# Performance work log

Hardware: AMD Instinct MI355X
Metric: run time of the kernel (lower is better)

## Reference

```python
import jax, jax.numpy as jnp
import numpy as np
import math

DIM = 1024
H = 16            # num_heads
HD = DIM // H // 2  # 32, per-split head dim
DEPTH = 4
LAMBDA_INIT = 0.8 - 0.6 * math.exp(-0.3 * DEPTH)
SCALE = HD ** -0.5
EPS = 1e-5


def setup_inputs() -> dict:
    key = jax.random.key(0)
    ks = jax.random.split(key, 12)
    B, Nq, Nk = 2, 2048, 2048
    s = DIM ** -0.5
    return {
        "query": jax.random.normal(ks[0], (B, Nq, DIM), jnp.float32),
        "key_": jax.random.normal(ks[1], (B, Nk, DIM), jnp.float32),
        "value": jax.random.normal(ks[2], (B, Nk, DIM), jnp.float32),
        "Wq": jax.random.normal(ks[3], (DIM, DIM), jnp.float32) * s,
        "Wk": jax.random.normal(ks[4], (DIM, DIM), jnp.float32) * s,
        "Wv": jax.random.normal(ks[5], (DIM, DIM), jnp.float32) * s,
        "Wp": jax.random.normal(ks[6], (DIM, DIM), jnp.float32) * s,
        "bp": jnp.zeros((DIM,), jnp.float32),
        "lq1": jax.random.normal(ks[7], (HD,), jnp.float32) * 0.1,
        "lk1": jax.random.normal(ks[8], (HD,), jnp.float32) * 0.1,
        "lq2": jax.random.normal(ks[9], (HD,), jnp.float32) * 0.1,
        "lk2": jax.random.normal(ks[10], (HD,), jnp.float32) * 0.1,
        "subln_w": jnp.ones((2 * HD,), jnp.float32),
    }


def _sdpa(q, k, v):
    # q,k: [B,H,Nq/Nk,HD], v: [B,H,Nk,2*HD]
    scores = jnp.einsum("bhqd,bhkd->bhqk", q * SCALE, k)
    p = jax.nn.softmax(scores, axis=-1)
    return jnp.einsum("bhqk,bhkd->bhqd", p, v)


def reference(query, key_, value, Wq, Wk, Wv, Wp, bp, lq1, lk1, lq2, lk2, subln_w):
    B, Nq, C = query.shape
    Nk = key_.shape[1]
    # projections (torch Linear: x @ W.T)
    q = (query @ Wq.T).reshape(B, Nq, 2 * H, HD).transpose(0, 2, 1, 3)  # [B,2H,Nq,HD]
    k = (key_ @ Wk.T).reshape(B, Nk, 2 * H, HD).transpose(0, 2, 1, 3)   # [B,2H,Nk,HD]
    v = (value @ Wv.T).reshape(B, Nk, H, 2 * HD).transpose(0, 2, 1, 3)  # [B,H,Nk,2HD]
    q1, q2 = q[:, :H], q[:, H:]
    k1, k2 = k[:, :H], k[:, H:]
    a1 = _sdpa(q1, k1, v)  # [B,H,Nq,2HD]
    a2 = _sdpa(q2, k2, v)
    lam1 = jnp.exp(jnp.sum(lq1 * lk1))
    lam2 = jnp.exp(jnp.sum(lq2 * lk2))
    lam = lam1 - lam2 + LAMBDA_INIT
    attn = a1 - lam * a2                       # [B,H,Nq,2HD]
    attn = attn.transpose(0, 2, 1, 3)          # [B,Nq,H,2HD]
    # RMSNorm over last dim
    attn = attn * jax.lax.rsqrt(jnp.mean(attn * attn, axis=-1, keepdims=True) + EPS)
    attn = attn * subln_w
    attn = attn * (1.0 - LAMBDA_INIT)
    attn = attn.reshape(B, Nq, C)
    return attn @ Wp.T + bp
```

## Files before the change

kernel.cpp:

```cpp
#include <hip/hip_runtime.h>

using u16 = unsigned short;
using u32 = unsigned int;
typedef __attribute__((ext_vector_type(8))) short bf16x8;
typedef __attribute__((ext_vector_type(4))) float f32x4;
typedef __attribute__((ext_vector_type(4))) float f4;

#define DIMC 1024
#define NQ 2048
#define NK 2048

static constexpr float LAMBDA_INIT = 0.6192834728526787f;
static constexpr float ONE_MINUS_LI = 1.0f - 0.6192834728526787f;
static constexpr float SCALE_ = 0.17677669529663687f;
static constexpr float LOG2E_ = 1.4426950408889634f;
static constexpr float EPS_ = 1e-5f;

__device__ __forceinline__ u16 f2bf(float f) {
    union { float f; unsigned u; } v; v.f = f;
    unsigned u = v.u;
    unsigned r = (u + 0x7FFFu + ((u >> 16) & 1u)) >> 16;
    return (u16)r;
}

__device__ __forceinline__ u32 packbf_trunc(float a, float b) {
    return (__float_as_uint(a) >> 16) | (__float_as_uint(b) & 0xFFFF0000u);
}

__device__ __forceinline__ void gload_lds16(const u16* g, u16* l) {
    __builtin_amdgcn_global_load_lds(
        (const __attribute__((address_space(1))) unsigned int*)g,
        (__attribute__((address_space(3))) unsigned int*)l,
        16, 0, 0);
}

__global__ __launch_bounds__(256) void cvt_all_kernel(
    const float* __restrict__ q, const float* __restrict__ k, const float* __restrict__ v,
    const float* __restrict__ wq, const float* __restrict__ wk,
    const float* __restrict__ wv, const float* __restrict__ wp,
    u16* __restrict__ qo, u16* __restrict__ ko, u16* __restrict__ vo,
    u16* __restrict__ wqo, u16* __restrict__ wko, u16* __restrict__ wvo, u16* __restrict__ wpo)
{
    const int bid = blockIdx.x;
    const float* s; u16* d; int rb;
    if (bid < 6144) {
        const int r = bid >> 11;
        rb = bid & 2047;
        s = (r == 0) ? q : (r == 1) ? k : v;
        d = (r == 0) ? qo : (r == 1) ? ko : vo;
    } else {
        const int r = (bid - 6144) >> 9;
        rb = (bid - 6144) & 511;
        s = (r == 0) ? wq : (r == 1) ? wk : (r == 2) ? wv : wp;
        d = (r == 0) ? wqo : (r == 1) ? wko : (r == 2) ? wvo : wpo;
    }
    const size_t i = (size_t)rb * 2048 + threadIdx.x * 8;
    f4 a = *(const f4*)(s + i);
    f4 b = *(const f4*)(s + i + 4);
    bf16x8 r8;
    r8[0] = (short)f2bf(a[0]); r8[1] = (short)f2bf(a[1]);
    r8[2] = (short)f2bf(a[2]); r8[3] = (short)f2bf(a[3]);
    r8[4] = (short)f2bf(b[0]); r8[5] = (short)f2bf(b[1]);
    r8[6] = (short)f2bf(b[2]); r8[7] = (short)f2bf(b[3]);
    *(bf16x8*)(d + i) = r8;
}

template<int OUT_MODE>
__device__ __forceinline__ void gemm_tile(
    const u16* __restrict__ A, const u16* __restrict__ B,
    void* __restrict__ C, const float* __restrict__ bias,
    int tm, int tn, int N, float osc)
{
    constexpr int K = 1024;
    const int lane = threadIdx.x & 63;
    const int wave = threadIdx.x >> 6;
    const int wr = wave >> 1, wc = wave & 1;
    const int l15 = lane & 15, l4 = lane >> 4;
    const int arow0 = tm + wr * 64, brow0 = tn + wc * 64;

    const u16* Ab = A + (size_t)(arow0 + l15) * K + 8 * l4;
    const u16* Bb = B + (size_t)(brow0 + l15) * K + 8 * l4;

    f32x4 acc[4][4];
    f32x4 zf = {0.f, 0.f, 0.f, 0.f};
#pragma unroll
    for (int i = 0; i < 4; ++i)
#pragma unroll
        for (int j = 0; j < 4; ++j) acc[i][j] = zf;

#pragma unroll 2
    for (int k0 = 0; k0 < K; k0 += 32) {
        bf16x8 af[4], bfr[4];
#pragma unroll
        for (int i = 0; i < 4; ++i) af[i] = *(const bf16x8*)(Ab + (size_t)i * 16 * K + k0);
#pragma unroll
        for (int j = 0; j < 4; ++j) bfr[j] = *(const bf16x8*)(Bb + (size_t)j * 16 * K + k0);
#pragma unroll
        for (int i = 0; i < 4; ++i)
#pragma unroll
            for (int j = 0; j < 4; ++j)
                acc[i][j] = __builtin_amdgcn_mfma_f32_16x16x32_bf16(af[i], bfr[j], acc[i][j], 0, 0, 0);
    }

#pragma unroll
    for (int i = 0; i < 4; ++i)
#pragma unroll
        for (int j = 0; j < 4; ++j)
#pragma unroll
            for (int r = 0; r < 4; ++r) {
                const int row = arow0 + i * 16 + l4 * 4 + r;
                const int col = brow0 + j * 16 + l15;
                const float v = acc[i][j][r];
                if (OUT_MODE == 0)
                    ((u16*)C)[(size_t)row * N + col] = f2bf(v * osc);
                else
                    ((float*)C)[(size_t)row * N + col] = v + bias[col];
            }
}

__global__ __launch_bounds__(256) void qkv_gemm_kernel(
    const u16* __restrict__ qa, const u16* __restrict__ wq, u16* __restrict__ qo,
    const u16* __restrict__ ka, const u16* __restrict__ wk, u16* __restrict__ ko,
    const u16* __restrict__ wv, const u16* __restrict__ va, u16* __restrict__ vo,
    float qosc)
{
    int id = blockIdx.x + 8 * (blockIdx.y + 32 * blockIdx.z);
    id = (id & 7) * 96 + (id >> 3);
    const int x = id & 7, y = (id >> 3) & 31, z = id >> 8;

    if (z == 0)      gemm_tile<0>(qa, wq, qo, nullptr, y * 128, x * 128, 1024, qosc);
    else if (z == 1) gemm_tile<0>(ka, wk, ko, nullptr, y * 128, x * 128, 1024, 1.0f);
    else             gemm_tile<0>(wv, va, vo, nullptr, x * 128, y * 128, 4096, 1.0f);
}

__global__ __launch_bounds__(256) void out_gemm_kernel(
    const u16* __restrict__ A, const u16* __restrict__ Bw,
    float* __restrict__ C, const float* __restrict__ bias)
{
    int id = blockIdx.x + 8 * blockIdx.y;
    id = (id & 7) * 32 + (id >> 3);
    const int x = id & 7, y = id >> 3;
    gemm_tile<1>(A, Bw, C, bias, y * 128, x * 128, 1024, 1.0f);
}

__global__ __launch_bounds__(256) void attn_kernel(
    const u16* __restrict__ Qb, const u16* __restrict__ Kb, const u16* __restrict__ Vt,
    const float* __restrict__ lq1, const float* __restrict__ lk1,
    const float* __restrict__ lq2, const float* __restrict__ lk2,
    const float* __restrict__ subln, u16* __restrict__ X2)
{
    const int tid = threadIdx.x;
    const int lane = tid & 63;
    const int wv = tid >> 6;
    const int l15 = lane & 15, l4 = lane >> 4;

    int id = blockIdx.x;
    id = (id & 7) * 128 + (id >> 3);
    const int qt = id & 31, h = (id >> 5) & 15, b = id >> 9;
    const int q0 = qt * 64 + wv * 16;

    __shared__ alignas(16) u16 Kbuf[2][4096];
    __shared__ alignas(16) u16 Vbuf[2][4096];
    __shared__ alignas(16) u16 Ps[4][2][1024];
    u16* P1 = &Ps[wv][0][0];
    u16* P2 = &Ps[wv][1][0];

    float s1 = 0.f, s2 = 0.f;
#pragma unroll
    for (int i = 0; i < 32; ++i) { s1 += lq1[i] * lk1[i]; s2 += lq2[i] * lk2[i]; }
    const float lam = __expf(s1) - __expf(s2) + LAMBDA_INIT;

    const u16* Qbase = Qb + (size_t)b * NQ * DIMC;
    const u16* Krow = Kb + (size_t)b * NK * DIMC + (size_t)lane * DIMC + h * 32;
    const u16* Vrow = Vt + (size_t)h * 64 * 4096 + (size_t)b * 2048 + (size_t)lane * 4096;

    const bf16x8 q1f = *(const bf16x8*)(Qbase + (size_t)(q0 + l15) * DIMC + h * 32 + 8 * l4);
    const bf16x8 q2f = *(const bf16x8*)(Qbase + (size_t)(q0 + l15) * DIMC + 512 + h * 32 + 8 * l4);

    float m1 = -1e30f, d1 = 0.f, m2 = -1e30f, d2 = 0.f;
    f32x4 acc1[4], acc2[4];
    f32x4 zf = {0.f, 0.f, 0.f, 0.f};
#pragma unroll
    for (int t = 0; t < 4; ++t) { acc1[t] = zf; acc2[t] = zf; }

    const int wrow = l4 << 2;

    auto STAGE = [&](int nb, int kv) {
#pragma unroll
        for (int g = 0; g < 2; ++g) {
            const int c = g * 4 + wv;
            const int koff = (c < 4) ? c * 8 : 512 + (c - 4) * 8;
            gload_lds16(Krow + (size_t)kv * DIMC + koff, &Kbuf[nb][c * 512]);
            gload_lds16(Vrow + kv + c * 8,               &Vbuf[nb][c * 512]);
        }
    };

    STAGE(0, 0);
    __syncthreads();

    int buf = 0;
    for (int t = 0; t < 32; ++t) {
        if (t < 31) STAGE(buf ^ 1, (t + 1) * 64);

        const u16* Kl = &Kbuf[buf][0];
        const u16* Vl = &Vbuf[buf][0];

        f32x4 sc1[4], sc2[4];
#pragma unroll
        for (int s = 0; s < 4; ++s) {
            bf16x8 k1 = *(const bf16x8*)(Kl + l4 * 512 + (s * 16 + l15) * 8);
            bf16x8 k2 = *(const bf16x8*)(Kl + (4 + l4) * 512 + (s * 16 + l15) * 8);
            sc1[s] = __builtin_amdgcn_mfma_f32_16x16x32_bf16(k1, q1f, zf, 0, 0, 0);
            sc2[s] = __builtin_amdgcn_mfma_f32_16x16x32_bf16(k2, q2f, zf, 0, 0, 0);
        }

        {
            float pm = sc1[0][0];
#pragma unroll
            for (int s = 0; s < 4; ++s)
#pragma unroll
                for (int r = 0; r < 4; ++r) pm = fmaxf(pm, sc1[s][r]);
            pm = fmaxf(pm, __shfl_xor(pm, 16));
            pm = fmaxf(pm, __shfl_xor(pm, 32));
            if (!__all(pm - m1 <= 8.f)) {
                const float mnew = fmaxf(m1, pm);
                const float alpha = __builtin_amdgcn_exp2f(m1 - mnew);
                m1 = mnew;
                d1 *= alpha;
                float ar[4];
#pragma unroll
                for (int r = 0; r < 4; ++r) ar[r] = __shfl(alpha, wrow + r);
#pragma unroll
                for (int tt = 0; tt < 4; ++tt)
#pragma unroll
                    for (int r = 0; r < 4; ++r) acc1[tt][r] *= ar[r];
            }
            float rs = 0.f;
            float p[4][4];
#pragma unroll
            for (int s = 0; s < 4; ++s)
#pragma unroll
                for (int r = 0; r < 4; ++r) {
                    p[s][r] = __builtin_amdgcn_exp2f(sc1[s][r] - m1);
                    rs += p[s][r];
                }
            rs += __shfl_xor(rs, 16);
            rs += __shfl_xor(rs, 32);
            d1 += rs;
#pragma unroll
            for (int s = 0; s < 4; ++s) {
                uint2 wvv;
                wvv.x = packbf_trunc(p[s][0], p[s][1]);
                wvv.y = packbf_trunc(p[s][2], p[s][3]);
                const int idx = ((l15 << 6) + (s << 4) + (l4 << 2)) ^ ((l15 & 7) << 3);
                *(uint2*)&P1[idx] = wvv;
            }
        }
        {
            float pm = sc2[0][0];
#pragma unroll
            for (int s = 0; s < 4; ++s)
#pragma unroll
                for (int r = 0; r < 4; ++r) pm = fmaxf(pm, sc2[s][r]);
            pm = fmaxf(pm, __shfl_xor(pm, 16));
            pm = fmaxf(pm, __shfl_xor(pm, 32));
            if (!__all(pm - m2 <= 8.f)) {
                const float mnew = fmaxf(m2, pm);
                const float alpha = __builtin_amdgcn_exp2f(m2 - mnew);
                m2 = mnew;
                d2 *= alpha;
                float ar[4];
#pragma unroll
                for (int r = 0; r < 4; ++r) ar[r] = __shfl(alpha, wrow + r);
#pragma unroll
                for (int tt = 0; tt < 4; ++tt)
#pragma unroll
                    for (int r = 0; r < 4; ++r) acc2[tt][r] *= ar[r];
            }
            float rs = 0.f;
            float p[4][4];
#pragma unroll
            for (int s = 0; s < 4; ++s)
#pragma unroll
                for (int r = 0; r < 4; ++r) {
                    p[s][r] = __builtin_amdgcn_exp2f(sc2[s][r] - m2);
                    rs += p[s][r];
                }
            rs += __shfl_xor(rs, 16);
            rs += __shfl_xor(rs, 32);
            d2 += rs;
#pragma unroll
            for (int s = 0; s < 4; ++s) {
                uint2 wvv;
                wvv.x = packbf_trunc(p[s][0], p[s][1]);
                wvv.y = packbf_trunc(p[s][2], p[s][3]);
                const int idx = ((l15 << 6) + (s << 4) + (l4 << 2)) ^ ((l15 & 7) << 3);
                *(uint2*)&P2[idx] = wvv;
            }
        }

#pragma unroll
        for (int kc = 0; kc < 2; ++kc) {
            const int ridx = ((l15 << 6) + (kc << 5) + (l4 << 3)) ^ ((l15 & 7) << 3);
            const bf16x8 p1a = *(const bf16x8*)&P1[ridx];
            const bf16x8 p2a = *(const bf16x8*)&P2[ridx];
#pragma unroll
            for (int tt = 0; tt < 4; ++tt) {
                bf16x8 vb = *(const bf16x8*)(Vl + (kc * 4 + l4) * 512 + (tt * 16 + l15) * 8);
                acc1[tt] = __builtin_amdgcn_mfma_f32_16x16x32_bf16(p1a, vb, acc1[tt], 0, 0, 0);
                acc2[tt] = __builtin_amdgcn_mfma_f32_16x16x32_bf16(p2a, vb, acc2[tt], 0, 0, 0);
            }
        }

        __syncthreads();
        buf ^= 1;
    }

    float i1[4], i2[4];
#pragma unroll
    for (int r = 0; r < 4; ++r) {
        i1[r] = 1.f / __shfl(d1, wrow + r);
        i2[r] = 1.f / __shfl(d2, wrow + r);
    }

    float vals[4][4];
    float ss[4] = {0.f, 0.f, 0.f, 0.f};
#pragma unroll
    for (int t = 0; t < 4; ++t)
#pragma unroll
        for (int r = 0; r < 4; ++r) {
            const float v = acc1[t][r] * i1[r] - lam * (acc2[t][r] * i2[r]);
            vals[t][r] = v;
            ss[r] += v * v;
        }
#pragma unroll
    for (int r = 0; r < 4; ++r) {
        float s = ss[r];
        s += __shfl_xor(s, 1); s += __shfl_xor(s, 2);
        s += __shfl_xor(s, 4); s += __shfl_xor(s, 8);
        ss[r] = rsqrtf(s * (1.f / 64.f) + EPS_) * ONE_MINUS_LI;
    }
#pragma unroll
    for (int t = 0; t < 4; ++t)
#pragma unroll
        for (int r = 0; r < 4; ++r) {
            const int col = t * 16 + l15;
            const int row = q0 + wrow + r;
            const float o = vals[t][r] * ss[r] * subln[col];
            X2[(size_t)(b * NQ + row) * DIMC + h * 64 + col] = f2bf(o);
        }
}

extern "C" void kernel_launch(void* const* d_in, const int* in_sizes, int n_in,
                              void* d_out, int out_size, void* d_ws, size_t ws_size,
                              hipStream_t stream) {
    const float* query = (const float*)d_in[0];
    const float* key_  = (const float*)d_in[1];
    const float* value = (const float*)d_in[2];
    const float* Wq    = (const float*)d_in[3];
    const float* Wk    = (const float*)d_in[4];
    const float* Wv    = (const float*)d_in[5];
    const float* Wp    = (const float*)d_in[6];
    const float* bp    = (const float*)d_in[7];
    const float* lq1   = (const float*)d_in[8];
    const float* lk1   = (const float*)d_in[9];
    const float* lq2   = (const float*)d_in[10];
    const float* lk2   = (const float*)d_in[11];
    const float* subln = (const float*)d_in[12];
    float* out = (float*)d_out;

    const size_t MB4 = (size_t)4096 * 1024;
    const size_t MB1 = (size_t)1024 * 1024;
    u16* base = (u16*)d_ws;
    u16* qbf = base;
    u16* kbf = qbf + MB4;
    u16* vbf = kbf + MB4;
    u16* wqb = vbf + MB4;
    u16* wkb = wqb + MB1;
    u16* wvb = wkb + MB1;
    u16* wpb = wvb + MB1;
    u16* Qb  = wpb + MB1;
    u16* Kb  = Qb + MB4;
    u16* Vt  = Kb + MB4;
    u16* X2  = vbf;

    dim3 bb(256, 1, 1);
    hipLaunchKernelGGL(cvt_all_kernel, dim3(8192), bb, 0, stream,
                       query, key_, value, Wq, Wk, Wv, Wp,
                       qbf, kbf, vbf, wqb, wkb, wvb, wpb);

    hipLaunchKernelGGL(qkv_gemm_kernel, dim3(8, 32, 3), bb, 0, stream,
                       qbf, wqb, Qb, kbf, wkb, Kb, wvb, vbf, Vt, SCALE_ * LOG2E_);

    hipLaunchKernelGGL(attn_kernel, dim3(1024), bb, 0, stream,
                       Qb, Kb, Vt, lq1, lk1, lq2, lk2, subln, X2);

    hipLaunchKernelGGL(out_gemm_kernel, dim3(8, 32, 1), bb, 0, stream, X2, wpb, out, bp);
}
```

Measured before the change: 385.3 us.

## Stage GEMM operand tiles through double-buffered LDS with async global loads

The projection and output GEMMs previously read A/B fragments directly from global memory into registers each k-step. They now copy 128x32 tiles of A and B into double-buffered shared memory using direct global-to-LDS loads (gload_lds16), prefetching the next k-tile while MFMAs consume the current one. This is meant to overlap memory latency with compute and coalesce loads across the block. The cost is 32 KB of LDS per block and a block-wide barrier every k-step. Correctness depends on gload_lds16 completing before the barrier, and the compact LDS layout may cause bank conflicts on fragment reads.

New measurement: 334.6 us. 1.15x faster.

```diff
diff --git a/kernel.cpp b/kernel.cpp
--- a/kernel.cpp
+++ b/kernel.cpp
@@ -66,20 +66,29 @@
 }
 
 template<int OUT_MODE>
-__device__ __forceinline__ void gemm_tile(
+__device__ __forceinline__ void gemm_tile_staged(
+    u16 (*Ab)[4096], u16 (*Bb)[4096],
     const u16* __restrict__ A, const u16* __restrict__ B,
     void* __restrict__ C, const float* __restrict__ bias,
     int tm, int tn, int N, float osc)
 {
     constexpr int K = 1024;
-    const int lane = threadIdx.x & 63;
-    const int wave = threadIdx.x >> 6;
-    const int wr = wave >> 1, wc = wave & 1;
+    const int tid = threadIdx.x;
+    const int lane = tid & 63;
+    const int wv = tid >> 6;
+    const int wr = wv >> 1, wc = wv & 1;
     const int l15 = lane & 15, l4 = lane >> 4;
-    const int arow0 = tm + wr * 64, brow0 = tn + wc * 64;
-
-    const u16* Ab = A + (size_t)(arow0 + l15) * K + 8 * l4;
-    const u16* Bb = B + (size_t)(brow0 + l15) * K + 8 * l4;
+
+    auto STAGE = [&](int nb, int k0) {
+#pragma unroll
+        for (int g = 0; g < 2; ++g) {
+            const int sbase = g * 256 + wv * 64;
+            const int slot = sbase + lane;
+            const int c = slot >> 7, row = slot & 127;
+            gload_lds16(A + (size_t)(tm + row) * K + k0 + c * 8, &Ab[nb][sbase * 8]);
+            gload_lds16(B + (size_t)(tn + row) * K + k0 + c * 8, &Bb[nb][sbase * 8]);
+        }
+    };
 
     f32x4 acc[4][4];
     f32x4 zf = {0.f, 0.f, 0.f, 0.f};
@@ -88,18 +97,28 @@
 #pragma unroll
         for (int j = 0; j < 4; ++j) acc[i][j] = zf;
 
-#pragma unroll 2
-    for (int k0 = 0; k0 < K; k0 += 32) {
+    STAGE(0, 0);
+    __syncthreads();
+
+    int buf = 0;
+    for (int t = 0; t < 32; ++t) {
+        if (t < 31) STAGE(buf ^ 1, (t + 1) * 32);
+
         bf16x8 af[4], bfr[4];
 #pragma unroll
-        for (int i = 0; i < 4; ++i) af[i] = *(const bf16x8*)(Ab + (size_t)i * 16 * K + k0);
-#pragma unroll
-        for (int j = 0; j < 4; ++j) bfr[j] = *(const bf16x8*)(Bb + (size_t)j * 16 * K + k0);
+        for (int i = 0; i < 4; ++i)
+            af[i] = *(const bf16x8*)&Ab[buf][l4 * 1024 + (wr * 64 + i * 16 + l15) * 8];
+#pragma unroll
+        for (int j = 0; j < 4; ++j)
+            bfr[j] = *(const bf16x8*)&Bb[buf][l4 * 1024 + (wc * 64 + j * 16 + l15) * 8];
 #pragma unroll
         for (int i = 0; i < 4; ++i)
 #pragma unroll
             for (int j = 0; j < 4; ++j)
                 acc[i][j] = __builtin_amdgcn_mfma_f32_16x16x32_bf16(af[i], bfr[j], acc[i][j], 0, 0, 0);
+
+        __syncthreads();
+        buf ^= 1;
     }
 
 #pragma unroll
@@ -108,8 +127,8 @@
         for (int j = 0; j < 4; ++j)
 #pragma unroll
             for (int r = 0; r < 4; ++r) {
-                const int row = arow0 + i * 16 + l4 * 4 + r;
-                const int col = brow0 + j * 16 + l15;
+                const int row = tm + wr * 64 + i * 16 + l4 * 4 + r;
+                const int col = tn + wc * 64 + j * 16 + l15;
                 const float v = acc[i][j][r];
                 if (OUT_MODE == 0)
                     ((u16*)C)[(size_t)row * N + col] = f2bf(v * osc);
@@ -124,23 +143,29 @@
     const u16* __restrict__ wv, const u16* __restrict__ va, u16* __restrict__ vo,
     float qosc)
 {
+    __shared__ alignas(16) u16 Ab[2][4096];
+    __shared__ alignas(16) u16 Bb[2][4096];
+
     int id = blockIdx.x + 8 * (blockIdx.y + 32 * blockIdx.z);
     id = (id & 7) * 96 + (id >> 3);
     const int x = id & 7, y = (id >> 3) & 31, z = id >> 8;
 
-    if (z == 0)      gemm_tile<0>(qa, wq, qo, nullptr, y * 128, x * 128, 1024, qosc);
-    else if (z == 1) gemm_tile<0>(ka, wk, ko, nullptr, y * 128, x * 128, 1024, 1.0f);
-    else             gemm_tile<0>(wv, va, vo, nullptr, x * 128, y * 128, 4096, 1.0f);
+    if (z == 0)      gemm_tile_staged<0>(Ab, Bb, qa, wq, qo, nullptr, y * 128, x * 128, 1024, qosc);
+    else if (z == 1) gemm_tile_staged<0>(Ab, Bb, ka, wk, ko, nullptr, y * 128, x * 128, 1024, 1.0f);
+    else             gemm_tile_staged<0>(Ab, Bb, wv, va, vo, nullptr, x * 128, y * 128, 4096, 1.0f);
 }
 
 __global__ __launch_bounds__(256) void out_gemm_kernel(
     const u16* __restrict__ A, const u16* __restrict__ Bw,
     float* __restrict__ C, const float* __restrict__ bias)
 {
+    __shared__ alignas(16) u16 Ab[2][4096];
+    __shared__ alignas(16) u16 Bb[2][4096];
+
     int id = blockIdx.x + 8 * blockIdx.y;
     id = (id & 7) * 32 + (id >> 3);
     const int x = id & 7, y = id >> 3;
-    gemm_tile<1>(A, Bw, C, bias, y * 128, x * 128, 1024, 1.0f);
+    gemm_tile_staged<1>(Ab, Bb, A, Bw, C, bias, y * 128, x * 128, 1024, 1.0f);
 }
 
 __global__ __launch_bounds__(256) void attn_kernel(
```
